# Performance work log

Hardware: AMD Instinct MI355X
Metric: run time of the kernel (lower is better)

## Reference

```python
import jax, jax.numpy as jnp
import numpy as np

N_NODES = 65536
N_EDGES = 524288
N_LAYERS = 3
D = 128
ED = 32
BATCH = 64
NEG_SLOPE = 0.2


def setup_inputs() -> dict:
    key = jax.random.key(0)
    ks = jax.random.split(key, 10)
    w_scale = 1.0 / np.sqrt(D)
    return {
        "x": jax.random.normal(ks[0], (N_NODES, D), dtype=jnp.float32),
        "edge_index": jax.random.randint(ks[1], (2, N_EDGES), 0, N_NODES, dtype=jnp.int32),
        "edge_attr": jax.random.normal(ks[2], (N_EDGES, ED), dtype=jnp.float32),
        "Ws": jax.random.normal(ks[3], (N_LAYERS, D, D), dtype=jnp.float32) * w_scale,
        "att_src": jax.random.normal(ks[4], (N_LAYERS, D), dtype=jnp.float32) * w_scale,
        "att_dst": jax.random.normal(ks[5], (N_LAYERS, D), dtype=jnp.float32) * w_scale,
        "W_edge": jax.random.normal(ks[6], (N_LAYERS, ED, D), dtype=jnp.float32) * (1.0 / np.sqrt(ED)),
        "att_edge": jax.random.normal(ks[7], (N_LAYERS, D), dtype=jnp.float32) * w_scale,
        "bias": jnp.zeros((N_LAYERS, D), dtype=jnp.float32),
        "batch_size": BATCH,
    }


def _gat_layer(x, src, dst, ea, W, a_s, a_d, We, a_e, b, n):
    # PyG GATConv, heads=1, concat=True, flow source_to_target.
    h = x @ W                                      # [N, D]
    al = (h @ a_s)[src] + (h @ a_d)[dst] + (ea @ We) @ a_e   # [E]
    al = jax.nn.leaky_relu(al, NEG_SLOPE)
    # segment softmax over destination-node neighborhoods
    m = jax.ops.segment_max(al, dst, num_segments=n)
    ex = jnp.exp(al - m[dst])
    den = jax.ops.segment_sum(ex, dst, num_segments=n)
    w = ex / den[dst]                              # [E]
    out = jax.ops.segment_sum(w[:, None] * h[src], dst, num_segments=n)
    return out + b


def reference(x, edge_index, edge_attr, Ws, att_src, att_dst, W_edge, att_edge, bias, batch_size):
    n = x.shape[0]
    # add_self_loops with fill_value='mean': self-loop edge_attr is the mean of
    # incoming edge features per destination node (zero if no incoming edges).
    loop = jnp.arange(n, dtype=edge_index.dtype)
    src = jnp.concatenate([edge_index[0], loop])
    dst = jnp.concatenate([edge_index[1], loop])
    cnt = jax.ops.segment_sum(jnp.ones((edge_attr.shape[0],), edge_attr.dtype), edge_index[1], num_segments=n)
    fill = jax.ops.segment_sum(edge_attr, edge_index[1], num_segments=n) / jnp.maximum(cnt, 1.0)[:, None]
    ea = jnp.concatenate([edge_attr, fill], axis=0)

    h = x
    for l in range(Ws.shape[0]):
        h = jax.nn.gelu(
            _gat_layer(h, src, dst, ea, Ws[l], att_src[l], att_dst[l], W_edge[l], att_edge[l], bias[l], n),
            approximate=False,
        )
        # dropout p=0.2 is identity in eval mode
    return h.reshape(batch_size, n // batch_size, -1)
```

## Files before the change

### kernel.cpp

```cpp
#include <hip/hip_runtime.h>
#include <math.h>

#define NN 65536
#define NE 524288
#define D 128
#define ED 32
#define NEG_SLOPE 0.2f

typedef short bf16x8 __attribute__((ext_vector_type(8)));
typedef float f32x4 __attribute__((ext_vector_type(4)));

__device__ __forceinline__ float leaky(float x) { return x > 0.f ? x : NEG_SLOPE * x; }
__device__ __forceinline__ float gelu_exact(float x) {
    return 0.5f * x * (1.f + erff(x * 0.70710678118654752440f));
}
__device__ __forceinline__ unsigned short bf16_rne(float x) {
    unsigned u = __float_as_uint(x);
    return (unsigned short)((u + 0x7FFFu + ((u >> 16) & 1u)) >> 16);
}


__global__ void k_hist(const int* __restrict__ dst, int* __restrict__ deg) {
    int e = blockIdx.x * 256 + threadIdx.x;
    atomicAdd(&deg[dst[e]], 1);
}

__global__ void k_scan1(const int* __restrict__ deg, int* __restrict__ rp, int* __restrict__ bsum) {
    __shared__ int s[256];
    int t = threadIdx.x;
    int i = blockIdx.x * 256 + t;
    int v = deg[i];
    s[t] = v;
    __syncthreads();
    #pragma unroll
    for (int off = 1; off < 256; off <<= 1) {
        int x = (t >= off) ? s[t - off] : 0;
        __syncthreads();
        s[t] += x;
        __syncthreads();
    }
    rp[i] = s[t] - v;
    if (t == 255) bsum[blockIdx.x] = s[t];
}

__global__ void k_scan2(const int* __restrict__ bsum, int* __restrict__ bscan, int* __restrict__ rp) {
    __shared__ int s[256];
    int t = threadIdx.x;
    int v = bsum[t];
    s[t] = v;
    __syncthreads();
    #pragma unroll
    for (int off = 1; off < 256; off <<= 1) {
        int x = (t >= off) ? s[t - off] : 0;
        __syncthreads();
        s[t] += x;
        __syncthreads();
    }
    bscan[t] = s[t] - v;
    if (t == 255) rp[NN] = s[t];
}

__global__ void k_scan3(int* __restrict__ rp, const int* __restrict__ bscan, int* __restrict__ cursor) {
    int i = blockIdx.x * 256 + threadIdx.x;
    int v = rp[i] + bscan[blockIdx.x];
    rp[i] = v;
    cursor[i] = v;
}


__global__ void k_wvec(const float* __restrict__ We, const float* __restrict__ ae, float* __restrict__ wvec) {
    int t = threadIdx.x;
    if (t < 3 * ED) {
        int l = t / ED, k = t % ED;
        const float* w = We + (long)(l * ED + k) * D;
        const float* a = ae + (long)l * D;
        float s = 0.f;
        #pragma unroll
        for (int i = 0; i < D; ++i) s += w[i] * a[i];
        wvec[t] = s;
    }
}

__global__ void k_scatter_ale(const int* __restrict__ srcArr, const int* __restrict__ dstArr,
                              int* __restrict__ cursor, const float* __restrict__ ea,
                              const float* __restrict__ wvec, int4* __restrict__ edata) {
    int e = blockIdx.x * 256 + threadIdx.x;
    int d = dstArr[e];
    int p = atomicAdd(&cursor[d], 1);
    const float4* row = (const float4*)(ea + (long)e * ED);
    const float4* w0 = (const float4*)(wvec);
    const float4* w1 = (const float4*)(wvec + ED);
    const float4* w2 = (const float4*)(wvec + 2 * ED);
    float s0 = 0.f, s1 = 0.f, s2 = 0.f;
    #pragma unroll
    for (int i = 0; i < ED / 4; ++i) {
        float4 v = row[i];
        float4 a = w0[i], b = w1[i], c = w2[i];
        s0 += v.x * a.x + v.y * a.y + v.z * a.z + v.w * a.w;
        s1 += v.x * b.x + v.y * b.y + v.z * b.z + v.w * b.w;
        s2 += v.x * c.x + v.y * c.y + v.z * c.z + v.w * c.w;
    }
    edata[p] = make_int4(srcArr[e], __float_as_int(s0), __float_as_int(s1), __float_as_int(s2));
}

__global__ void k_wpack(const float* __restrict__ Ws, short* __restrict__ Whp, short* __restrict__ Wlp) {
    int t = blockIdx.x * 256 + threadIdx.x;
    if (t >= 3 * 4 * 4 * 128) return;
    int n = t & 127;
    int q = (t >> 7) & 3;
    int ks = (t >> 9) & 3;
    int l = t >> 11;
    const float* w = Ws + (size_t)l * D * D;
    size_t obase = (size_t)l * D * D + ((size_t)((ks * 4 + q) * 128) + n) * 8;
    #pragma unroll
    for (int j = 0; j < 8; ++j) {
        float x = w[(size_t)(ks * 32 + q * 8 + j) * D + n];
        unsigned short hb = bf16_rne(x);
        float hf = __uint_as_float(((unsigned)hb) << 16);
        Whp[obase + j] = (short)hb;
        Wlp[obase + j] = (short)bf16_rne(x - hf);
    }
}

__global__ void k_splitx(const float* __restrict__ x, unsigned short* __restrict__ Hh,
                         unsigned short* __restrict__ Hl) {
    int i = blockIdx.x * 256 + threadIdx.x;
    float4 v = ((const float4*)x)[i];
    float xs[4] = {v.x, v.y, v.z, v.w};
    ushort4 h, l;
    unsigned short* hp = (unsigned short*)&h;
    unsigned short* lp = (unsigned short*)&l;
    #pragma unroll
    for (int j = 0; j < 4; ++j) {
        unsigned short hb = bf16_rne(xs[j]);
        float hf = __uint_as_float(((unsigned)hb) << 16);
        hp[j] = hb;
        lp[j] = bf16_rne(xs[j] - hf);
    }
    ((ushort4*)Hh)[i] = h;
    ((ushort4*)Hl)[i] = l;
}


__global__ __launch_bounds__(256) void k_gemm_mfma(const unsigned short* __restrict__ Ah,
        const unsigned short* __restrict__ Al,
        const short* __restrict__ Whp, const short* __restrict__ Wlp,
        const float* __restrict__ a_s, const float* __restrict__ a_d,
        float* __restrict__ C, float* __restrict__ als, float* __restrict__ ald) {
    int t = threadIdx.x;
    int wave = t >> 6, lane = t & 63;
    int l16 = lane & 15, q = lane >> 4;
    int rows_base = blockIdx.x * 128 + wave * 32;

    f32x4 acc[2][8] = {};
    #pragma unroll
    for (int ks = 0; ks < 4; ++ks) {
        bf16x8 ah[2], alo[2];
        #pragma unroll
        for (int mt = 0; mt < 2; ++mt) {
            size_t abase = (size_t)(rows_base + mt * 16 + l16) * D + ks * 32 + q * 8;
            ah[mt]  = *(const bf16x8*)(Ah + abase);
            alo[mt] = *(const bf16x8*)(Al + abase);
        }
        #pragma unroll
        for (int nt = 0; nt < 8; ++nt) {
            size_t idx = ((size_t)((ks * 4 + q) * 128) + nt * 16 + l16) * 8;
            bf16x8 bh = *(const bf16x8*)(Whp + idx);
            bf16x8 bl = *(const bf16x8*)(Wlp + idx);
            #pragma unroll
            for (int mt = 0; mt < 2; ++mt) {
                acc[mt][nt] = __builtin_amdgcn_mfma_f32_16x16x32_bf16(ah[mt], bh, acc[mt][nt], 0, 0, 0);
                acc[mt][nt] = __builtin_amdgcn_mfma_f32_16x16x32_bf16(ah[mt], bl, acc[mt][nt], 0, 0, 0);
                acc[mt][nt] = __builtin_amdgcn_mfma_f32_16x16x32_bf16(alo[mt], bh, acc[mt][nt], 0, 0, 0);
            }
        }
    }

    float as_r[8], ad_r[8];
    #pragma unroll
    for (int nt = 0; nt < 8; ++nt) {
        int col = nt * 16 + l16;
        as_r[nt] = a_s[col];
        ad_r[nt] = a_d[col];
    }
    #pragma unroll
    for (int mt = 0; mt < 2; ++mt) {
        #pragma unroll
        for (int r = 0; r < 4; ++r) {
            int row = rows_base + mt * 16 + q * 4 + r;
            float ps = 0.f, pd = 0.f;
            #pragma unroll
            for (int nt = 0; nt < 8; ++nt) {
                float v = acc[mt][nt][r];
                ps += v * as_r[nt];
                pd += v * ad_r[nt];
                C[(size_t)row * D + nt * 16 + l16] = v;
            }
            #pragma unroll
            for (int off = 8; off >= 1; off >>= 1) {
                ps += __shfl_xor(ps, off);
                pd += __shfl_xor(pd, off);
            }
            if (l16 == 0) {
                als[row] = ps;
                ald[row] = pd;
            }
        }
    }
}

__global__ __launch_bounds__(256) void k_aggr_fused(const float* __restrict__ h,
        const float* __restrict__ als, const float* __restrict__ ald,
        const int4* __restrict__ edata, const int* __restrict__ rp,
        const float* __restrict__ bias, int lsel, float* __restrict__ out_f32,
        unsigned* __restrict__ out_hi, unsigned* __restrict__ out_lo) {
    int wave = threadIdx.x >> 6, lane = threadIdx.x & 63;
    int n = blockIdx.x * 4 + wave;
    int s = rp[n], e = rp[n + 1];
    int deg = e - s;
    float aldd = ald[n];
    float alsn = als[n];
    float inv_deg = (deg > 0) ? 1.f / (float)deg : 0.f;

    float2 hv = ((const float2*)(h + (size_t)n * D))[lane];
    float ax, ay;

    if (deg <= 64) {
        int sn0 = 0;
        float al0 = -1e30f, alev0 = 0.f;
        if (lane < deg) {
            int4 ed = edata[s + lane];
            sn0 = ed.x;
            int ai = (lsel == 0) ? ed.y : ((lsel == 1) ? ed.z : ed.w);
            alev0 = __int_as_float(ai);
            al0 = leaky(als[sn0] + aldd + alev0);
        }
        float m = al0, asum = alev0;
        #pragma unroll
        for (int off = 1; off < 64; off <<= 1) {
            m = fmaxf(m, __shfl_xor(m, off));
            asum += __shfl_xor(asum, off);
        }
        float self_al = leaky(alsn + aldd + asum * inv_deg);
        m = fmaxf(m, self_al);
        float p0 = (lane < deg) ? __expf(al0 - m) : 0.f;
        float den = p0;
        #pragma unroll
        for (int off = 1; off < 64; off <<= 1) den += __shfl_xor(den, off);
        float es = __expf(self_al - m);
        den += es;
        float inv = 1.f / den;
        float w0 = p0 * inv;
        float wself = es * inv;

        ax = wself * hv.x;
        ay = wself * hv.y;
        int t = 0;
        for (; t + 8 <= deg; t += 8) {
            int   sA = __shfl(sn0, t),     sB = __shfl(sn0, t + 1), sC = __shfl(sn0, t + 2), sD = __shfl(sn0, t + 3);
            int   sE = __shfl(sn0, t + 4), sF = __shfl(sn0, t + 5), sG = __shfl(sn0, t + 6), sH = __shfl(sn0, t + 7);
            float wA = __shfl(w0, t),      wB = __shfl(w0, t + 1),  wC = __shfl(w0, t + 2),  wD = __shfl(w0, t + 3);
            float wE = __shfl(w0, t + 4),  wF = __shfl(w0, t + 5),  wG = __shfl(w0, t + 6),  wH = __shfl(w0, t + 7);
            float2 hA = ((const float2*)(h + (size_t)sA * D))[lane];
            float2 hB = ((const float2*)(h + (size_t)sB * D))[lane];
            float2 hC = ((const float2*)(h + (size_t)sC * D))[lane];
            float2 hD = ((const float2*)(h + (size_t)sD * D))[lane];
            float2 hE = ((const float2*)(h + (size_t)sE * D))[lane];
            float2 hF = ((const float2*)(h + (size_t)sF * D))[lane];
            float2 hG = ((const float2*)(h + (size_t)sG * D))[lane];
            float2 hH = ((const float2*)(h + (size_t)sH * D))[lane];
            ax += wA * hA.x + wB * hB.x + wC * hC.x + wD * hD.x + wE * hE.x + wF * hF.x + wG * hG.x + wH * hH.x;
            ay += wA * hA.y + wB * hB.y + wC * hC.y + wD * hD.y + wE * hE.y + wF * hF.y + wG * hG.y + wH * hH.y;
        }
        for (; t + 4 <= deg; t += 4) {
            int   sA = __shfl(sn0, t), sB = __shfl(sn0, t + 1), sC = __shfl(sn0, t + 2), sD = __shfl(sn0, t + 3);
            float wA = __shfl(w0, t),  wB = __shfl(w0, t + 1),  wC = __shfl(w0, t + 2),  wD = __shfl(w0, t + 3);
            float2 hA = ((const float2*)(h + (size_t)sA * D))[lane];
            float2 hB = ((const float2*)(h + (size_t)sB * D))[lane];
            float2 hC = ((const float2*)(h + (size_t)sC * D))[lane];
            float2 hD = ((const float2*)(h + (size_t)sD * D))[lane];
            ax += wA * hA.x + wB * hB.x + wC * hC.x + wD * hD.x;
            ay += wA * hA.y + wB * hB.y + wC * hC.y + wD * hD.y;
        }
        for (; t < deg; ++t) {
            int st = __shfl(sn0, t);
            float wt = __shfl(w0, t);
            float2 ht = ((const float2*)(h + (size_t)st * D))[lane];
            ax += wt * ht.x;
            ay += wt * ht.y;
        }
    } else {
        float m = -1e30f, asum = 0.f;
        for (int base = s; base < e; base += 64) {
            int j = base + lane;
            if (j < e) {
                int4 ed = edata[j];
                int ai = (lsel == 0) ? ed.y : ((lsel == 1) ? ed.z : ed.w);
                float alev = __int_as_float(ai);
                asum += alev;
                m = fmaxf(m, leaky(als[ed.x] + aldd + alev));
            }
        }
        #pragma unroll
        for (int off = 1; off < 64; off <<= 1) {
            m = fmaxf(m, __shfl_xor(m, off));
            asum += __shfl_xor(asum, off);
        }
        float self_al = leaky(alsn + aldd + asum * inv_deg);
        m = fmaxf(m, self_al);
        float den = 0.f;
        for (int base = s; base < e; base += 64) {
            int j = base + lane;
            if (j < e) {
                int4 ed = edata[j];
                int ai = (lsel == 0) ? ed.y : ((lsel == 1) ? ed.z : ed.w);
                den += __expf(leaky(als[ed.x] + aldd + __int_as_float(ai)) - m);
            }
        }
        #pragma unroll
        for (int off = 1; off < 64; off <<= 1) den += __shfl_xor(den, off);
        float es = __expf(self_al - m);
        den += es;
        float inv = 1.f / den;
        float wself = es * inv;
        ax = wself * hv.x;
        ay = wself * hv.y;
        for (int base = s; base < e; base += 64) {
            int cnt = min(e - base, 64);
            int sn = 0;
            float w = 0.f;
            if (lane < cnt) {
                int4 ed = edata[base + lane];
                sn = ed.x;
                int ai = (lsel == 0) ? ed.y : ((lsel == 1) ? ed.z : ed.w);
                w = __expf(leaky(als[sn] + aldd + __int_as_float(ai)) - m) * inv;
            }
            for (int t = 0; t < cnt; ++t) {
                int st = __shfl(sn, t);
                float wt = __shfl(w, t);
                float2 ht = ((const float2*)(h + (size_t)st * D))[lane];
                ax += wt * ht.x;
                ay += wt * ht.y;
            }
        }
    }

    float2 b2 = ((const float2*)bias)[lane];
    float ox = gelu_exact(ax + b2.x);
    float oy = gelu_exact(ay + b2.y);
    if (out_f32) {
        ((float2*)(out_f32 + (size_t)n * D))[lane] = make_float2(ox, oy);
    } else {
        unsigned short h0 = bf16_rne(ox);
        float h0f = __uint_as_float(((unsigned)h0) << 16);
        unsigned short l0 = bf16_rne(ox - h0f);
        unsigned short h1 = bf16_rne(oy);
        float h1f = __uint_as_float(((unsigned)h1) << 16);
        unsigned short l1 = bf16_rne(oy - h1f);
        out_hi[(size_t)n * 64 + lane] = (unsigned)h0 | ((unsigned)h1 << 16);
        out_lo[(size_t)n * 64 + lane] = (unsigned)l0 | ((unsigned)l1 << 16);
    }
}


extern "C" void kernel_launch(void* const* d_in, const int* in_sizes, int n_in,
                              void* d_out, int out_size, void* d_ws, size_t ws_size,
                              hipStream_t stream) {
    (void)in_sizes; (void)n_in; (void)out_size; (void)ws_size;
    const float* x        = (const float*)d_in[0];
    const int*   eidx     = (const int*)d_in[1];
    const float* ea       = (const float*)d_in[2];
    const float* Ws       = (const float*)d_in[3];
    const float* att_src  = (const float*)d_in[4];
    const float* att_dst  = (const float*)d_in[5];
    const float* W_edge   = (const float*)d_in[6];
    const float* att_edge = (const float*)d_in[7];
    const float* bias     = (const float*)d_in[8];
    float* out = (float*)d_out;

    char* ws = (char*)d_ws;
    size_t off = 0;
    auto alloc = [&](size_t bytes) {
        void* p = ws + off;
        off += (bytes + 255) & ~(size_t)255;
        return p;
    };
    float*          B0   = (float*)alloc((size_t)NN * D * 4);
    unsigned short* Hh   = (unsigned short*)alloc((size_t)NN * D * 2);
    unsigned short* Hl   = (unsigned short*)alloc((size_t)NN * D * 2);
    float*          als  = (float*)alloc((size_t)NN * 4);
    float*          ald  = (float*)alloc((size_t)NN * 4);
    int4*           edata= (int4*)alloc((size_t)NE * 16);
    float*          wvec = (float*)alloc(3 * ED * 4);
    int*            deg  = (int*)alloc((size_t)NN * 4);
    int*            rp   = (int*)alloc((size_t)(NN + 4) * 4);
    int*            cursor = (int*)alloc((size_t)NN * 4);
    int*            bsum = (int*)alloc(256 * 4);
    int*            bscan= (int*)alloc(256 * 4);
    short*          Whp  = (short*)alloc((size_t)3 * D * D * 2);
    short*          Wlp  = (short*)alloc((size_t)3 * D * D * 2);

    const int* e_src = eidx;
    const int* e_dst = eidx + NE;

    hipMemsetAsync(deg, 0, (size_t)NN * 4, stream);
    k_hist<<<NE / 256, 256, 0, stream>>>(e_dst, deg);
    k_scan1<<<NN / 256, 256, 0, stream>>>(deg, rp, bsum);
    k_scan2<<<1, 256, 0, stream>>>(bsum, bscan, rp);
    k_scan3<<<NN / 256, 256, 0, stream>>>(rp, bscan, cursor);

    k_wvec<<<1, 128, 0, stream>>>(W_edge, att_edge, wvec);
    k_scatter_ale<<<NE / 256, 256, 0, stream>>>(e_src, e_dst, cursor, ea, wvec, edata);
    k_wpack<<<24, 256, 0, stream>>>(Ws, Whp, Wlp);
    k_splitx<<<(NN * D / 4) / 256, 256, 0, stream>>>(x, Hh, Hl);

    for (int l = 0; l < 3; ++l) {
        k_gemm_mfma<<<NN / 128, 256, 0, stream>>>(Hh, Hl, Whp + (size_t)l * D * D, Wlp + (size_t)l * D * D,
                                                  att_src + (size_t)l * D, att_dst + (size_t)l * D,
                                                  B0, als, ald);
        bool last = (l == 2);
        k_aggr_fused<<<NN / 4, 256, 0, stream>>>(B0, als, ald, edata, rp, bias + (size_t)l * D, l,
                                                 last ? out : nullptr,
                                                 (unsigned*)Hh, (unsigned*)Hl);
    }
}
```

Before: 423.2 us.

## Store projected features as bf16 and aggregate with 16 lanes per node

The GEMM now writes the projected features h as bf16 instead of fp32, halving the bytes gathered per neighbor in the aggregation kernel. The aggregation maps one node to 16 lanes, each loading 8 bf16 values in a single 16-byte load, so four nodes share a wave and the grid shrinks accordingly. The GEMM also stages its weight tiles in LDS in two halves rather than reading them from global memory per wave. Rounding h to bf16 before the weighted sum adds precision loss, and degrees above 16 now take the slower multi-pass path.

```diff
diff --git a/kernel.cpp b/kernel.cpp
--- a/kernel.cpp
+++ b/kernel.cpp
@@ -9,6 +9,7 @@
 
 typedef short bf16x8 __attribute__((ext_vector_type(8)));
 typedef float f32x4 __attribute__((ext_vector_type(4)));
+typedef unsigned short ushort_t;
 
 __device__ __forceinline__ float leaky(float x) { return x > 0.f ? x : NEG_SLOPE * x; }
 __device__ __forceinline__ float gelu_exact(float x) {
@@ -17,6 +18,13 @@
 __device__ __forceinline__ unsigned short bf16_rne(float x) {
     unsigned u = __float_as_uint(x);
     return (unsigned short)((u + 0x7FFFu + ((u >> 16) & 1u)) >> 16);
+}
+__device__ __forceinline__ void unpack8(int4 r, float* f) {
+    unsigned u0 = (unsigned)r.x, u1 = (unsigned)r.y, u2 = (unsigned)r.z, u3 = (unsigned)r.w;
+    f[0] = __uint_as_float(u0 << 16); f[1] = __uint_as_float(u0 & 0xFFFF0000u);
+    f[2] = __uint_as_float(u1 << 16); f[3] = __uint_as_float(u1 & 0xFFFF0000u);
+    f[4] = __uint_as_float(u2 << 16); f[5] = __uint_as_float(u2 & 0xFFFF0000u);
+    f[6] = __uint_as_float(u3 << 16); f[7] = __uint_as_float(u3 & 0xFFFF0000u);
 }
 
 
@@ -122,14 +130,14 @@
     }
 }
 
-__global__ void k_splitx(const float* __restrict__ x, unsigned short* __restrict__ Hh,
-                         unsigned short* __restrict__ Hl) {
+__global__ void k_splitx(const float* __restrict__ x, ushort_t* __restrict__ Hh,
+                         ushort_t* __restrict__ Hl) {
     int i = blockIdx.x * 256 + threadIdx.x;
     float4 v = ((const float4*)x)[i];
     float xs[4] = {v.x, v.y, v.z, v.w};
     ushort4 h, l;
-    unsigned short* hp = (unsigned short*)&h;
-    unsigned short* lp = (unsigned short*)&l;
+    ushort_t* hp = (ushort_t*)&h;
+    ushort_t* lp = (ushort_t*)&l;
     #pragma unroll
     for (int j = 0; j < 4; ++j) {
         unsigned short hb = bf16_rne(xs[j]);
@@ -142,36 +150,54 @@
 }
 
 
-__global__ __launch_bounds__(256) void k_gemm_mfma(const unsigned short* __restrict__ Ah,
-        const unsigned short* __restrict__ Al,
+__global__ __launch_bounds__(256) void k_gemm_mfma(const ushort_t* __restrict__ Ah,
+        const ushort_t* __restrict__ Al,
         const short* __restrict__ Whp, const short* __restrict__ Wlp,
         const float* __restrict__ a_s, const float* __restrict__ a_d,
-        float* __restrict__ C, float* __restrict__ als, float* __restrict__ ald) {
+        ushort_t* __restrict__ Hb, float* __restrict__ als, float* __restrict__ ald) {
+    __shared__ int4 BsH[1024];
+    __shared__ int4 BsL[1024];
     int t = threadIdx.x;
     int wave = t >> 6, lane = t & 63;
     int l16 = lane & 15, q = lane >> 4;
     int rows_base = blockIdx.x * 128 + wave * 32;
 
+    const int4* wh4 = (const int4*)Whp;
+    const int4* wl4 = (const int4*)Wlp;
+    const short* bsh = (const short*)BsH;
+    const short* bsl = (const short*)BsL;
+
     f32x4 acc[2][8] = {};
     #pragma unroll
-    for (int ks = 0; ks < 4; ++ks) {
-        bf16x8 ah[2], alo[2];
-        #pragma unroll
-        for (int mt = 0; mt < 2; ++mt) {
-            size_t abase = (size_t)(rows_base + mt * 16 + l16) * D + ks * 32 + q * 8;
-            ah[mt]  = *(const bf16x8*)(Ah + abase);
-            alo[mt] = *(const bf16x8*)(Al + abase);
-        }
-        #pragma unroll
-        for (int nt = 0; nt < 8; ++nt) {
-            size_t idx = ((size_t)((ks * 4 + q) * 128) + nt * 16 + l16) * 8;
-            bf16x8 bh = *(const bf16x8*)(Whp + idx);
-            bf16x8 bl = *(const bf16x8*)(Wlp + idx);
+    for (int h2 = 0; h2 < 2; ++h2) {
+        if (h2) __syncthreads();
+        #pragma unroll
+        for (int i = 0; i < 4; ++i) {
+            BsH[t + 256 * i] = wh4[h2 * 1024 + t + 256 * i];
+            BsL[t + 256 * i] = wl4[h2 * 1024 + t + 256 * i];
+        }
+        __syncthreads();
+        #pragma unroll
+        for (int kk = 0; kk < 2; ++kk) {
+            int ks = h2 * 2 + kk;
+            bf16x8 ah[2], alo[2];
             #pragma unroll
             for (int mt = 0; mt < 2; ++mt) {
-                acc[mt][nt] = __builtin_amdgcn_mfma_f32_16x16x32_bf16(ah[mt], bh, acc[mt][nt], 0, 0, 0);
-                acc[mt][nt] = __builtin_amdgcn_mfma_f32_16x16x32_bf16(ah[mt], bl, acc[mt][nt], 0, 0, 0);
-                acc[mt][nt] = __builtin_amdgcn_mfma_f32_16x16x32_bf16(alo[mt], bh, acc[mt][nt], 0, 0, 0);
+                size_t abase = (size_t)(rows_base + mt * 16 + l16) * D + ks * 32 + q * 8;
+                ah[mt]  = *(const bf16x8*)(Ah + abase);
+                alo[mt] = *(const bf16x8*)(Al + abase);
+            }
+            #pragma unroll
+            for (int nt = 0; nt < 8; ++nt) {
+                int idx = (((kk * 4 + q) * 128) + nt * 16 + l16) * 8;
+                bf16x8 bh = *(const bf16x8*)(bsh + idx);
+                bf16x8 bl = *(const bf16x8*)(bsl + idx);
+                #pragma unroll
+                for (int mt = 0; mt < 2; ++mt) {
+                    acc[mt][nt] = __builtin_amdgcn_mfma_f32_16x16x32_bf16(ah[mt], bh, acc[mt][nt], 0, 0, 0);
+                    acc[mt][nt] = __builtin_amdgcn_mfma_f32_16x16x32_bf16(ah[mt], bl, acc[mt][nt], 0, 0, 0);
+                    acc[mt][nt] = __builtin_amdgcn_mfma_f32_16x16x32_bf16(alo[mt], bh, acc[mt][nt], 0, 0, 0);
+                }
             }
         }
     }
@@ -194,7 +220,7 @@
                 float v = acc[mt][nt][r];
                 ps += v * as_r[nt];
                 pd += v * ad_r[nt];
-                C[(size_t)row * D + nt * 16 + l16] = v;
+                Hb[(size_t)row * D + nt * 16 + l16] = bf16_rne(v);
             }
             #pragma unroll
             for (int off = 8; off >= 1; off >>= 1) {
@@ -209,156 +235,168 @@
     }
 }
 
-__global__ __launch_bounds__(256) void k_aggr_fused(const float* __restrict__ h,
+__global__ __launch_bounds__(256) void k_aggr_fused(const ushort_t* __restrict__ hb,
         const float* __restrict__ als, const float* __restrict__ ald,
         const int4* __restrict__ edata, const int* __restrict__ rp,
         const float* __restrict__ bias, int lsel, float* __restrict__ out_f32,
-        unsigned* __restrict__ out_hi, unsigned* __restrict__ out_lo) {
-    int wave = threadIdx.x >> 6, lane = threadIdx.x & 63;
-    int n = blockIdx.x * 4 + wave;
+        ushort_t* __restrict__ out_hi, ushort_t* __restrict__ out_lo) {
+    int t = threadIdx.x;
+    int lane = t & 63;
+    int l16 = lane & 15;
+    int qb = lane & 48;
+    int n = blockIdx.x * 16 + (t >> 4);
     int s = rp[n], e = rp[n + 1];
     int deg = e - s;
     float aldd = ald[n];
     float alsn = als[n];
     float inv_deg = (deg > 0) ? 1.f / (float)deg : 0.f;
 
-    float2 hv = ((const float2*)(h + (size_t)n * D))[lane];
-    float ax, ay;
-
-    if (deg <= 64) {
+    int4 hvp = *(const int4*)(hb + (size_t)n * D + l16 * 8);
+    float acc8[8];
+
+    if (deg <= 16) {
         int sn0 = 0;
         float al0 = -1e30f, alev0 = 0.f;
-        if (lane < deg) {
-            int4 ed = edata[s + lane];
+        if (l16 < deg) {
+            int4 ed = edata[s + l16];
             sn0 = ed.x;
-            int ai = (lsel == 0) ? ed.y : ((lsel == 1) ? ed.z : ed.w);
-            alev0 = __int_as_float(ai);
+            alev0 = __int_as_float((lsel == 0) ? ed.y : ((lsel == 1) ? ed.z : ed.w));
             al0 = leaky(als[sn0] + aldd + alev0);
         }
-        float m = al0, asum = alev0;
-        #pragma unroll
-        for (int off = 1; off < 64; off <<= 1) {
-            m = fmaxf(m, __shfl_xor(m, off));
+        float mm = al0, asum = alev0;
+        #pragma unroll
+        for (int off = 1; off < 16; off <<= 1) {
+            mm = fmaxf(mm, __shfl_xor(mm, off));
             asum += __shfl_xor(asum, off);
         }
         float self_al = leaky(alsn + aldd + asum * inv_deg);
-        m = fmaxf(m, self_al);
-        float p0 = (lane < deg) ? __expf(al0 - m) : 0.f;
+        mm = fmaxf(mm, self_al);
+        float p0 = (l16 < deg) ? __expf(al0 - mm) : 0.f;
         float den = p0;
         #pragma unroll
-        for (int off = 1; off < 64; off <<= 1) den += __shfl_xor(den, off);
-        float es = __expf(self_al - m);
+        for (int off = 1; off < 16; off <<= 1) den += __shfl_xor(den, off);
+        float es = __expf(self_al - mm);
         den += es;
         float inv = 1.f / den;
         float w0 = p0 * inv;
         float wself = es * inv;
 
-        ax = wself * hv.x;
-        ay = wself * hv.y;
-        int t = 0;
-        for (; t + 8 <= deg; t += 8) {
-            int   sA = __shfl(sn0, t),     sB = __shfl(sn0, t + 1), sC = __shfl(sn0, t + 2), sD = __shfl(sn0, t + 3);
-            int   sE = __shfl(sn0, t + 4), sF = __shfl(sn0, t + 5), sG = __shfl(sn0, t + 6), sH = __shfl(sn0, t + 7);
-            float wA = __shfl(w0, t),      wB = __shfl(w0, t + 1),  wC = __shfl(w0, t + 2),  wD = __shfl(w0, t + 3);
-            float wE = __shfl(w0, t + 4),  wF = __shfl(w0, t + 5),  wG = __shfl(w0, t + 6),  wH = __shfl(w0, t + 7);
-            float2 hA = ((const float2*)(h + (size_t)sA * D))[lane];
-            float2 hB = ((const float2*)(h + (size_t)sB * D))[lane];
-            float2 hC = ((const float2*)(h + (size_t)sC * D))[lane];
-            float2 hD = ((const float2*)(h + (size_t)sD * D))[lane];
-            float2 hE = ((const float2*)(h + (size_t)sE * D))[lane];
-            float2 hF = ((const float2*)(h + (size_t)sF * D))[lane];
-            float2 hG = ((const float2*)(h + (size_t)sG * D))[lane];
-            float2 hH = ((const float2*)(h + (size_t)sH * D))[lane];
-            ax += wA * hA.x + wB * hB.x + wC * hC.x + wD * hD.x + wE * hE.x + wF * hF.x + wG * hG.x + wH * hH.x;
-            ay += wA * hA.y + wB * hB.y + wC * hC.y + wD * hD.y + wE * hE.y + wF * hF.y + wG * hG.y + wH * hH.y;
-        }
-        for (; t + 4 <= deg; t += 4) {
-            int   sA = __shfl(sn0, t), sB = __shfl(sn0, t + 1), sC = __shfl(sn0, t + 2), sD = __shfl(sn0, t + 3);
-            float wA = __shfl(w0, t),  wB = __shfl(w0, t + 1),  wC = __shfl(w0, t + 2),  wD = __shfl(w0, t + 3);
-            float2 hA = ((const float2*)(h + (size_t)sA * D))[lane];
-            float2 hB = ((const float2*)(h + (size_t)sB * D))[lane];
-            float2 hC = ((const float2*)(h + (size_t)sC * D))[lane];
-            float2 hD = ((const float2*)(h + (size_t)sD * D))[lane];
-            ax += wA * hA.x + wB * hB.x + wC * hC.x + wD * hD.x;
-            ay += wA * hA.y + wB * hB.y + wC * hC.y + wD * hD.y;
-        }
-        for (; t < deg; ++t) {
-            int st = __shfl(sn0, t);
-            float wt = __shfl(w0, t);
-            float2 ht = ((const float2*)(h + (size_t)st * D))[lane];
-            ax += wt * ht.x;
-            ay += wt * ht.y;
+        float fv[8];
+        unpack8(hvp, fv);
+        #pragma unroll
+        for (int j = 0; j < 8; ++j) acc8[j] = wself * fv[j];
+
+        int tt = 0;
+        for (; tt + 4 <= deg; tt += 4) {
+            int   sA = __shfl(sn0, qb + tt),     sB = __shfl(sn0, qb + tt + 1);
+            int   sC = __shfl(sn0, qb + tt + 2), sD = __shfl(sn0, qb + tt + 3);
+            float wA = __shfl(w0, qb + tt),      wB = __shfl(w0, qb + tt + 1);
+            float wC = __shfl(w0, qb + tt + 2),  wD = __shfl(w0, qb + tt + 3);
+            int4 rA = *(const int4*)(hb + (size_t)sA * D + l16 * 8);
+            int4 rB = *(const int4*)(hb + (size_t)sB * D + l16 * 8);
+            int4 rC = *(const int4*)(hb + (size_t)sC * D + l16 * 8);
+            int4 rD = *(const int4*)(hb + (size_t)sD * D + l16 * 8);
+            float fA[8], fB[8], fC[8], fD[8];
+            unpack8(rA, fA); unpack8(rB, fB); unpack8(rC, fC); unpack8(rD, fD);
+            #pragma unroll
+            for (int j = 0; j < 8; ++j)
+                acc8[j] += wA * fA[j] + wB * fB[j] + wC * fC[j] + wD * fD[j];
+        }
+        for (; tt < deg; ++tt) {
+            int st = __shfl(sn0, qb + tt);
+            float wt = __shfl(w0, qb + tt);
+            int4 r = *(const int4*)(hb + (size_t)st * D + l16 * 8);
+            float f[8];
+            unpack8(r, f);
+            #pragma unroll
+            for (int j = 0; j < 8; ++j) acc8[j] += wt * f[j];
         }
     } else {
-        float m = -1e30f, asum = 0.f;
-        for (int base = s; base < e; base += 64) {
-            int j = base + lane;
+        float mm = -1e30f, asum = 0.f;
+        for (int base = s; base < e; base += 16) {
+            int j = base + l16;
             if (j < e) {
                 int4 ed = edata[j];
-                int ai = (lsel == 0) ? ed.y : ((lsel == 1) ? ed.z : ed.w);
-                float alev = __int_as_float(ai);
+                float alev = __int_as_float((lsel == 0) ? ed.y : ((lsel == 1) ? ed.z : ed.w));
                 asum += alev;
-                m = fmaxf(m, leaky(als[ed.x] + aldd + alev));
-            }
-        }
-        #pragma unroll
-        for (int off = 1; off < 64; off <<= 1) {
-            m = fmaxf(m, __shfl_xor(m, off));
+                mm = fmaxf(mm, leaky(als[ed.x] + aldd + alev));
+            }
+        }
+        #pragma unroll
+        for (int off = 1; off < 16; off <<= 1) {
+            mm = fmaxf(mm, __shfl_xor(mm, off));
             asum += __shfl_xor(asum, off);
         }
         float self_al = leaky(alsn + aldd + asum * inv_deg);
-        m = fmaxf(m, self_al);
+        mm = fmaxf(mm, self_al);
         float den = 0.f;
-        for (int base = s; base < e; base += 64) {
-            int j = base + lane;
+        for (int base = s; base < e; base += 16) {
+            int j = base + l16;
             if (j < e) {
                 int4 ed = edata[j];
-                int ai = (lsel == 0) ? ed.y : ((lsel == 1) ? ed.z : ed.w);
-                den += __expf(leaky(als[ed.x] + aldd + __int_as_float(ai)) - m);
-            }
-        }
-        #pragma unroll
-        for (int off = 1; off < 64; off <<= 1) den += __shfl_xor(den, off);
-        float es = __expf(self_al - m);
+                float alev = __int_as_float((lsel == 0) ? ed.y : ((lsel == 1) ? ed.z : ed.w));
+                den += __expf(leaky(als[ed.x] + aldd + alev) - mm);
+            }
+        }
+        #pragma unroll
+        for (int off = 1; off < 16; off <<= 1) den += __shfl_xor(den, off);
+        float es = __expf(self_al - mm);
         den += es;
         float inv = 1.f / den;
         float wself = es * inv;
-        ax = wself * hv.x;
-        ay = wself * hv.y;
-        for (int base = s; base < e; base += 64) {
-            int cnt = min(e - base, 64);
+        float fv[8];
+        unpack8(hvp, fv);
+        #pragma unroll
+        for (int j = 0; j < 8; ++j) acc8[j] = wself * fv[j];
+        for (int base = s; base < e; base += 16) {
+            int cnt = min(e - base, 16);
             int sn = 0;
             float w = 0.f;
-            if (lane < cnt) {
-                int4 ed = edata[base + lane];
+            if (l16 < cnt) {
+                int4 ed = edata[base + l16];
                 sn = ed.x;
-                int ai = (lsel == 0) ? ed.y : ((lsel == 1) ? ed.z : ed.w);
-                w = __expf(leaky(als[sn] + aldd + __int_as_float(ai)) - m) * inv;
-            }
-            for (int t = 0; t < cnt; ++t) {
-                int st = __shfl(sn, t);
-                float wt = __shfl(w, t);
-                float2 ht = ((const float2*)(h + (size_t)st * D))[lane];
-                ax += wt * ht.x;
-                ay += wt * ht.y;
-            }
-        }
-    }
-
-    float2 b2 = ((const float2*)bias)[lane];
-    float ox = gelu_exact(ax + b2.x);
-    float oy = gelu_exact(ay + b2.y);
+                float alev = __int_as_float((lsel == 0) ? ed.y : ((lsel == 1) ? ed.z : ed.w));
+                w = __expf(leaky(als[sn] + aldd + alev) - mm) * inv;
+            }
+            for (int tt = 0; tt < cnt; ++tt) {
+                int st = __shfl(sn, qb + tt);
+                float wt = __shfl(w, qb + tt);
+                int4 r = *(const int4*)(hb + (size_t)st * D + l16 * 8);
+                float f[8];
+                unpack8(r, f);
+                #pragma unroll
+                for (int j = 0; j < 8; ++j) acc8[j] += wt * f[j];
+            }
+        }
+    }
+
+    const float4* b4 = (const float4*)(bias + l16 * 8);
+    float4 b0 = b4[0], b1 = b4[1];
+    float bb[8] = {b0.x, b0.y, b0.z, b0.w, b1.x, b1.y, b1.z, b1.w};
+    float o[8];
+    #pragma unroll
+    for (int j = 0; j < 8; ++j) o[j] = gelu_exact(acc8[j] + bb[j]);
+
     if (out_f32) {
-        ((float2*)(out_f32 + (size_t)n * D))[lane] = make_float2(ox, oy);
+        float4* o4 = (float4*)(out_f32 + (size_t)n * D + l16 * 8);
+        o4[0] = make_float4(o[0], o[1], o[2], o[3]);
+        o4[1] = make_float4(o[4], o[5], o[6], o[7]);
     } else {
-        unsigned short h0 = bf16_rne(ox);
-        float h0f = __uint_as_float(((unsigned)h0) << 16);
-        unsigned short l0 = bf16_rne(ox - h0f);
-        unsigned short h1 = bf16_rne(oy);
-        float h1f = __uint_as_float(((unsigned)h1) << 16);
-        unsigned short l1 = bf16_rne(oy - h1f);
-        out_hi[(size_t)n * 64 + lane] = (unsigned)h0 | ((unsigned)h1 << 16);
-        out_lo[(size_t)n * 64 + lane] = (unsigned)l0 | ((unsigned)l1 << 16);
+        ushort4 hi0, hi1, lo0, lo1;
+        ushort_t* h0p = (ushort_t*)&hi0; ushort_t* h1p = (ushort_t*)&hi1;
+        ushort_t* l0p = (ushort_t*)&lo0; ushort_t* l1p = (ushort_t*)&lo1;
+        #pragma unroll
+        for (int j = 0; j < 8; ++j) {
+            unsigned short hb16 = bf16_rne(o[j]);
+            float hf = __uint_as_float(((unsigned)hb16) << 16);
+            unsigned short lb16 = bf16_rne(o[j] - hf);
+            if (j < 4) { h0p[j] = hb16; l0p[j] = lb16; }
+            else       { h1p[j - 4] = hb16; l1p[j - 4] = lb16; }
+        }
+        ushort4* oh = (ushort4*)(out_hi + (size_t)n * D + l16 * 8);
+        ushort4* ol = (ushort4*)(out_lo + (size_t)n * D + l16 * 8);
+        oh[0] = hi0; oh[1] = hi1;
+        ol[0] = lo0; ol[1] = lo1;
     }
 }
 
@@ -385,20 +423,20 @@
         off += (bytes + 255) & ~(size_t)255;
         return p;
     };
-    float*          B0   = (float*)alloc((size_t)NN * D * 4);
-    unsigned short* Hh   = (unsigned short*)alloc((size_t)NN * D * 2);
-    unsigned short* Hl   = (unsigned short*)alloc((size_t)NN * D * 2);
-    float*          als  = (float*)alloc((size_t)NN * 4);
-    float*          ald  = (float*)alloc((size_t)NN * 4);
-    int4*           edata= (int4*)alloc((size_t)NE * 16);
-    float*          wvec = (float*)alloc(3 * ED * 4);
-    int*            deg  = (int*)alloc((size_t)NN * 4);
-    int*            rp   = (int*)alloc((size_t)(NN + 4) * 4);
-    int*            cursor = (int*)alloc((size_t)NN * 4);
-    int*            bsum = (int*)alloc(256 * 4);
-    int*            bscan= (int*)alloc(256 * 4);
-    short*          Whp  = (short*)alloc((size_t)3 * D * D * 2);
-    short*          Wlp  = (short*)alloc((size_t)3 * D * D * 2);
+    ushort_t* Hb   = (ushort_t*)alloc((size_t)NN * D * 2);
+    ushort_t* Hh   = (ushort_t*)alloc((size_t)NN * D * 2);
+    ushort_t* Hl   = (ushort_t*)alloc((size_t)NN * D * 2);
+    float*    als  = (float*)alloc((size_t)NN * 4);
+    float*    ald  = (float*)alloc((size_t)NN * 4);
+    int4*     edata= (int4*)alloc((size_t)NE * 16);
+    float*    wvec = (float*)alloc(3 * ED * 4);
+    int*      deg  = (int*)alloc((size_t)NN * 4);
+    int*      rp   = (int*)alloc((size_t)(NN + 4) * 4);
+    int*      cursor = (int*)alloc((size_t)NN * 4);
+    int*      bsum = (int*)alloc(256 * 4);
+    int*      bscan= (int*)alloc(256 * 4);
+    short*    Whp  = (short*)alloc((size_t)3 * D * D * 2);
+    short*    Wlp  = (short*)alloc((size_t)3 * D * D * 2);
 
     const int* e_src = eidx;
     const int* e_dst = eidx + NE;
@@ -417,10 +455,9 @@
     for (int l = 0; l < 3; ++l) {
         k_gemm_mfma<<<NN / 128, 256, 0, stream>>>(Hh, Hl, Whp + (size_t)l * D * D, Wlp + (size_t)l * D * D,
                                                   att_src + (size_t)l * D, att_dst + (size_t)l * D,
-                                                  B0, als, ald);
+                                                  Hb, als, ald);
         bool last = (l == 2);
-        k_aggr_fused<<<NN / 4, 256, 0, stream>>>(B0, als, ald, edata, rp, bias + (size_t)l * D, l,
-                                                 last ? out : nullptr,
-                                                 (unsigned*)Hh, (unsigned*)Hl);
-    }
-}
+        k_aggr_fused<<<NN / 16, 256, 0, stream>>>(Hb, als, ald, edata, rp, bias + (size_t)l * D, l,
+                                                  last ? out : nullptr, Hh, Hl);
+    }
+}
```

New measurement: 372.3 us. -12.0%, faster.
